# Kernel tuning notes

Hardware: AMD Instinct MI355X
Metric: run time of the kernel (lower is better)

The kernel has to match this reference:

```python
import jax, jax.numpy as jnp
import numpy as np

B, S, HID = 1, 2048, 2048
H, KVH, D = 16, 8, 128
QR, KR, VR = 6, 2, 2
SOFTCAP = 50.0
SCALING = D ** -0.5
NEG = -1e9


def _rope(Bfac, cos, sin):
    # Bfac: [b, s, r, d]; cos/sin: [s, d//2]; rotates adjacent pairs (complex view)
    x = Bfac.reshape(*Bfac.shape[:-1], D // 2, 2)
    xe, xo = x[..., 0], x[..., 1]
    c = cos[None, :, None, :]
    s = sin[None, :, None, :]
    oe = xe * c - xo * s
    oo = xe * s + xo * c
    return jnp.stack([oe, oo], axis=-1).reshape(Bfac.shape)


def setup_inputs() -> dict:
    key = jax.random.key(0)
    ks = jax.random.split(key, 12)
    hidden_states = jax.random.normal(ks[0], (B, S, HID), jnp.float32)
    # rotary tables (standard RoPE frequencies)
    inv_freq = 1.0 / (10000.0 ** (jnp.arange(0, D, 2, dtype=jnp.float32) / D))
    t = jnp.arange(S, dtype=jnp.float32)
    ang = t[:, None] * inv_freq[None, :]            # [S, D//2]
    cos, sin = jnp.cos(ang), jnp.sin(ang)
    # causal additive mask [1,1,S,S]
    causal = jnp.tril(jnp.ones((S, S), bool))
    mask = jnp.where(causal, 0.0, NEG).astype(jnp.float32)[None, None]
    kv_write_indices = jnp.arange(S, dtype=jnp.int32)
    sc = lambda k, shp: jax.random.normal(k, shp, jnp.float32) * (shp[0] ** -0.5)
    return {
        "hidden_states": hidden_states, "cos": cos, "sin": sin, "mask": mask,
        "kv_write_indices": kv_write_indices,
        "WAq": sc(ks[1], (HID, H * QR)), "WAk": sc(ks[2], (HID, KVH * KR)),
        "WAv": sc(ks[3], (HID, KVH * VR)), "WBq": sc(ks[4], (HID, QR * D)),
        "WBk": sc(ks[5], (HID, KR * D)), "WBv": sc(ks[6], (HID, VR * D)),
        "Wo": sc(ks[7], (H * D, HID)),
    }


def reference(hidden_states, cos, sin, mask, kv_write_indices,
              WAq, WAk, WAv, WBq, WBk, WBv, Wo):
    b, s, _ = hidden_states.shape
    # factor projections (never materialize full Q/K/V)
    A_q = (hidden_states @ WAq).reshape(b, s, H, QR)
    A_k = (hidden_states @ WAk).reshape(b, s, KVH, KR)
    A_v = (hidden_states @ WAv).reshape(b, s, KVH, VR)
    B_q = (hidden_states @ WBq).reshape(b, s, QR, D)
    B_k = (hidden_states @ WBk).reshape(b, s, KR, D)
    B_v = (hidden_states @ WBv).reshape(b, s, VR, D)
    # RoPE on B factors
    B_q = _rope(B_q, cos, sin)
    B_k = _rope(B_k, cos, sin)
    # prefill: kv_write_indices = arange(S) => cache slices equal current factors
    # GQA: broadcast KV heads up to H
    hpk = H // KVH
    A_k = jnp.repeat(A_k, hpk, axis=2)   # [b,k,H,KR]
    A_v = jnp.repeat(A_v, hpk, axis=2)   # [b,k,H,VR]
    # factor-expanded attention scores
    B_dots = jnp.einsum('bqrd,bksd->bqkrs', B_q, B_k) * SCALING
    attn = jnp.einsum('bqhr,bkhs,bqkrs->bhqk', A_q, A_k, B_dots)
    # logit softcapping
    attn = SOFTCAP * jnp.tanh(attn / SOFTCAP)
    attn = attn + mask
    probs = jax.nn.softmax(attn.astype(jnp.float32), axis=-1).astype(hidden_states.dtype)
    # factor-expanded output
    out = jnp.einsum('bhqk,bkhu,bkud->bhqd', probs, A_v, B_v)
    out = out.transpose(0, 2, 1, 3).reshape(b, s, H * D)
    return out @ Wo
```

## Files before the change

### kernel.cpp

```cpp
#include <hip/hip_runtime.h>


constexpr int SEQ   = 2048;
constexpr int HIDN  = 2048;
constexpr int NHEAD = 16;
constexpr int NKVH  = 8;
constexpr int DH    = 128;
constexpr int NCOLS = 1408;

typedef __bf16 bf16x8 __attribute__((ext_vector_type(8)));
typedef float  f32x4  __attribute__((ext_vector_type(4)));

#define MFMA(a, b, c) __builtin_amdgcn_mfma_f32_16x16x32_bf16((a), (b), (c), 0, 0, 0)

__device__ __forceinline__ void gload_lds16(const void* g, void* l) {
  __builtin_amdgcn_global_load_lds(
      (const __attribute__((address_space(1))) void*)g,
      (__attribute__((address_space(3))) void*)l, 16, 0, 0);
}


__global__ __launch_bounds__(256) void k_prep(
    const float* __restrict__ hidden,
    const float* __restrict__ WAq, const float* __restrict__ WAk,
    const float* __restrict__ WAv, const float* __restrict__ WBq,
    const float* __restrict__ WBk, const float* __restrict__ WBv,
    const float* __restrict__ Wo,
    __bf16* __restrict__ hid_bf, __bf16* __restrict__ WT,
    __bf16* __restrict__ WoT) {
  const int bid = blockIdx.x;
  if (bid < 2048) {
    const int i = (bid * 256 + threadIdx.x) * 8;
    f32x4 a = *(const f32x4*)(hidden + i);
    f32x4 b = *(const f32x4*)(hidden + i + 4);
    bf16x8 v;
#pragma unroll
    for (int j = 0; j < 4; j++) { v[j] = (__bf16)a[j]; v[4 + j] = (__bf16)b[j]; }
    *(bf16x8*)(hid_bf + i) = v;
  } else if (bid < 2048 + 44 * 64) {
    const int t = bid - 2048;
    const int bc = (t % 44) * 32, bk = (t / 44) * 32;
    __shared__ float tl[32][33];
    const int tx = threadIdx.x & 31, ty = threadIdx.x >> 5;
    const int c = bc + tx;
#pragma unroll
    for (int j = 0; j < 32; j += 8) {
      const int k = bk + ty + j;
      float v;
      if (c < 96)        v = WAq[k * 96 + c];
      else if (c < 112)  v = WAk[k * 16 + (c - 96)];
      else if (c < 128)  v = WAv[k * 16 + (c - 112)];
      else if (c < 896)  v = WBq[k * 768 + (c - 128)];
      else if (c < 1152) v = WBk[k * 256 + (c - 896)];
      else               v = WBv[k * 256 + (c - 1152)];
      tl[ty + j][tx] = v;
    }
    __syncthreads();
#pragma unroll
    for (int j = 0; j < 32; j += 8)
      WT[(size_t)(bc + ty + j) * HIDN + bk + tx] = (__bf16)tl[tx][ty + j];
  } else {
    const int t = bid - (2048 + 44 * 64);
    const int bn = (t % 64) * 32, bk = (t / 64) * 32;
    __shared__ float tl[32][33];
    const int tx = threadIdx.x & 31, ty = threadIdx.x >> 5;
#pragma unroll
    for (int j = 0; j < 32; j += 8)
      tl[ty + j][tx] = Wo[(size_t)(bk + ty + j) * HIDN + bn + tx];
    __syncthreads();
#pragma unroll
    for (int j = 0; j < 32; j += 8)
      WoT[(size_t)(bn + ty + j) * HIDN + bk + tx] = (__bf16)tl[tx][ty + j];
  }
}


__global__ __launch_bounds__(256) void k_gemm_bt(const __bf16* __restrict__ A,
                                                 const __bf16* __restrict__ BT,
                                                 float* __restrict__ C,
                                                 int M, int N, int K) {
  __shared__ __bf16 As[4][4096];
  __shared__ __bf16 Bs[4][2048];
  const int tid = threadIdx.x;
  const int w = tid >> 6, lane = tid & 63;
  const int lhi = lane >> 4, llo = lane & 15;
  const int wr = w >> 1, wc = w & 1;

  const int nx = gridDim.x, ny = gridDim.y;
  const int id = blockIdx.y * nx + blockIdx.x;
  int brow, bcol;
  if (((ny & 1) == 0) && ((nx & 3) == 0)) {
    const int g = id & 7, k = id >> 3;
    const int rows = ny >> 1, cols = nx >> 2;
    const int rg = g >> 2, cg = g & 3;
    const int r = k % rows, c = k / rows;
    brow = (rg * rows + r) * 128;
    bcol = (cg * cols + c) * 64;
  } else {
    const int cpx = (nx * ny) >> 3;
    const int sid = (id & 7) * cpx + (id >> 3);
    brow = (sid / nx) * 128;
    bcol = (sid % nx) * 64;
  }

  const int rA = lane >> 2, kA = (lane & 3) * 8;
  const int nt = K >> 5;

  f32x4 acc[4][2];
#pragma unroll
  for (int m = 0; m < 4; m++)
#pragma unroll
    for (int n = 0; n < 2; n++) acc[m][n] = (f32x4){0.f, 0.f, 0.f, 0.f};

  auto stage = [&](int t) {
    const int buf = t & 3;
    const int k0 = t * 32;
#pragma unroll
    for (int i = 0; i < 2; i++) {
      int seg = w * 2 + i;
      int row = seg * 16 + rA;
      gload_lds16(A + (size_t)(brow + row) * K + k0 + kA, &As[buf][seg * 512]);
    }
    gload_lds16(BT + (size_t)(bcol + w * 16 + rA) * K + k0 + kA, &Bs[buf][w * 512]);
  };

  stage(0); stage(1); stage(2);
  asm volatile("s_waitcnt vmcnt(6)" ::: "memory");
  __builtin_amdgcn_s_barrier();

  for (int t = 0; t < nt; t++) {
    if (t + 3 < nt) stage(t + 3);
    const int buf = t & 3;
    bf16x8 af[4], bfr[2];
#pragma unroll
    for (int m = 0; m < 4; m++)
      af[m] = *(const bf16x8*)&As[buf][(wr * 64 + m * 16 + llo) * 32 + lhi * 8];
#pragma unroll
    for (int n = 0; n < 2; n++)
      bfr[n] = *(const bf16x8*)&Bs[buf][(wc * 32 + n * 16 + llo) * 32 + lhi * 8];
#pragma unroll
    for (int m = 0; m < 4; m++)
#pragma unroll
      for (int n = 0; n < 2; n++) acc[m][n] = MFMA(af[m], bfr[n], acc[m][n]);
    const int rem = nt - 2 - t;
    if (rem >= 2)      asm volatile("s_waitcnt vmcnt(6)" ::: "memory");
    else if (rem == 1) asm volatile("s_waitcnt vmcnt(3)" ::: "memory");
    else               asm volatile("s_waitcnt vmcnt(0)" ::: "memory");
    __builtin_amdgcn_s_barrier();
  }

#pragma unroll
  for (int m = 0; m < 4; m++)
#pragma unroll
    for (int n = 0; n < 2; n++) {
      int r0 = brow + wr * 64 + m * 16 + lhi * 4;
      int c0 = bcol + wc * 32 + n * 16 + llo;
#pragma unroll
      for (int r = 0; r < 4; r++) C[(size_t)(r0 + r) * N + c0] = acc[m][n][r];
    }
}


__global__ __launch_bounds__(128) void k_build_qkv(const float* __restrict__ P,
                                                   const float* __restrict__ cosT,
                                                   const float* __restrict__ sinT,
                                                   __bf16* __restrict__ Qo,
                                                   __bf16* __restrict__ Ko,
                                                   __bf16* __restrict__ Vto) {
  const int q = blockIdx.x, d = threadIdx.x;
  __shared__ float Ash[128];
  const float* row = P + (size_t)q * NCOLS;
  Ash[d] = row[d];
  __syncthreads();
  const int m2 = (d >> 1) * 2;
  const bool odd = d & 1;
  const float c = cosT[q * 64 + (d >> 1)];
  const float s = sinT[q * 64 + (d >> 1)];

  float qacc[16];
#pragma unroll
  for (int h = 0; h < 16; h++) qacc[h] = 0.f;
#pragma unroll
  for (int r = 0; r < 6; r++) {
    float xe = row[128 + r * 128 + m2];
    float xo = row[128 + r * 128 + m2 + 1];
    float br = odd ? (xe * s + xo * c) : (xe * c - xo * s);
#pragma unroll
    for (int h = 0; h < 16; h++) qacc[h] += Ash[h * 6 + r] * br;
  }
#pragma unroll
  for (int h = 0; h < 16; h++)
    Qo[((size_t)h * SEQ + q) * DH + d] = (__bf16)(qacc[h] * 0.08838834764831845f);

  float kacc[8];
#pragma unroll
  for (int g = 0; g < 8; g++) kacc[g] = 0.f;
#pragma unroll
  for (int ss = 0; ss < 2; ss++) {
    float xe = row[896 + ss * 128 + m2];
    float xo = row[896 + ss * 128 + m2 + 1];
    float bs = odd ? (xe * s + xo * c) : (xe * c - xo * s);
#pragma unroll
    for (int g = 0; g < 8; g++) kacc[g] += Ash[96 + g * 2 + ss] * bs;
  }
#pragma unroll
  for (int g = 0; g < 8; g++)
    Ko[((size_t)g * SEQ + q) * DH + d] = (__bf16)kacc[g];

  float vacc[8];
#pragma unroll
  for (int g = 0; g < 8; g++) vacc[g] = 0.f;
#pragma unroll
  for (int u = 0; u < 2; u++) {
    float vu = row[1152 + u * 128 + d];
#pragma unroll
    for (int g = 0; g < 8; g++) vacc[g] += Ash[112 + g * 2 + u] * vu;
  }
#pragma unroll
  for (int g = 0; g < 8; g++)
    Vto[((size_t)g * DH + d) * SEQ + q] = (__bf16)vacc[g];
}


__global__ __launch_bounds__(256) void k_attn(const __bf16* __restrict__ Q,
                                              const __bf16* __restrict__ Kc,
                                              const __bf16* __restrict__ Vt,
                                              float* __restrict__ AOf0,
                                              float* __restrict__ AOf1,
                                              float* __restrict__ Ls) {
  const int raw = blockIdx.x;
  const int g = raw & 7;
  const int j = raw >> 3;
  const int bqi = 31 - (j >> 2);
  const int hh = (j >> 1) & 1;
  const int p = j & 1;
  const int h = g * 2 + hh;
  const int w = threadIdx.x >> 6, lane = threadIdx.x & 63;
  const int lhi = lane >> 4, llo = lane & 15;
  const int q0 = bqi * 64 + w * 16;
  const int t0 = p * (bqi + 1), t1 = t0 + bqi + 1;

  __shared__ __bf16 KVs[2][8192];
  __shared__ __bf16 Plds[4][512];

  const __bf16* Qh = Q  + (size_t)h * SEQ * DH;
  const __bf16* Kg = Kc + (size_t)g * SEQ * DH;
  const __bf16* Vg = Vt + (size_t)g * DH * SEQ;
  __bf16* Pl = Plds[w];
  float* AOc = p ? AOf1 : AOf0;

  bf16x8 aq[4];
#pragma unroll
  for (int c = 0; c < 4; c++)
    aq[c] = *(const bf16x8*)&Qh[(size_t)(q0 + llo) * DH + c * 32 + lhi * 8];

  f32x4 oacc[8];
  float lsum[4] = {0.f, 0.f, 0.f, 0.f};
#pragma unroll
  for (int n = 0; n < 8; n++) oacc[n] = (f32x4){0.f, 0.f, 0.f, 0.f};

  auto stage = [&](int kb, int buf) {
    __bf16* L = KVs[buf];
    if (w < 2) {
#pragma unroll
      for (int u = 0; u < 4; u++) {
        int c = w * 256 + u * 64 + lane;
        int row = c >> 4, jj = c & 15;
        gload_lds16(Kg + (size_t)(kb + row) * DH + ((jj ^ (row & 7)) * 8),
                    L + (w * 256 + u * 64) * 8);
      }
    } else {
#pragma unroll
      for (int u = 0; u < 4; u++) {
        int c = (w - 2) * 256 + u * 64 + lane;
        int d = c >> 2, jj = c & 3;
        gload_lds16(Vg + (size_t)d * SEQ + kb + ((jj ^ ((d >> 1) & 3)) * 8),
                    L + 4096 + ((w - 2) * 256 + u * 64) * 8);
      }
    }
  };

  stage(t0 * 32, t0 & 1);
  for (int t = t0; t < t1; t++) {
    const int kb = t * 32;
    const int buf = t & 1;
    if (t + 1 < t1) {
      stage(kb + 32, buf ^ 1);
      asm volatile("s_waitcnt vmcnt(4)" ::: "memory");
    } else {
      asm volatile("s_waitcnt vmcnt(0)" ::: "memory");
    }
    __builtin_amdgcn_s_barrier();
    if (kb <= q0 + 15) {
      const __bf16* Kl = KVs[buf];
      const __bf16* Vl = KVs[buf] + 4096;
      f32x4 s0 = {0.f, 0.f, 0.f, 0.f}, s1 = {0.f, 0.f, 0.f, 0.f};
#pragma unroll
      for (int c = 0; c < 4; c++) {
        const int row0 = llo, row1 = 16 + llo;
        bf16x8 k0 = *(const bf16x8*)((const char*)Kl + row0 * 256 +
                                     ((c * 64 + lhi * 16) ^ ((row0 & 7) << 4)));
        bf16x8 k1 = *(const bf16x8*)((const char*)Kl + row1 * 256 +
                                     ((c * 64 + lhi * 16) ^ ((row1 & 7) << 4)));
        s0 = MFMA(aq[c], k0, s0);
        s1 = MFMA(aq[c], k1, s1);
      }
#pragma unroll
      for (int r = 0; r < 4; r++) {
        const int qrow = q0 + lhi * 4 + r;
        const int rho = lhi * 4 + r;
        float t0e = exp2f(s0[r] * 0.057707802f);
        float t1e = exp2f(s1[r] * 0.057707802f);
        float p0 = exp2f(72.134752f - 144.269504f * __builtin_amdgcn_rcpf(t0e + 1.f));
        float p1 = exp2f(72.134752f - 144.269504f * __builtin_amdgcn_rcpf(t1e + 1.f));
        if (kb + llo > qrow) p0 = 0.f;
        if (kb + 16 + llo > qrow) p1 = 0.f;
        lsum[r] += p0 + p1;
        const int sw = ((rho >> 1) & 3) << 4;
        *(__bf16*)((char*)Pl + rho * 64 + ((llo * 2) ^ sw))      = (__bf16)p0;
        *(__bf16*)((char*)Pl + rho * 64 + ((llo * 2 + 32) ^ sw)) = (__bf16)p1;
      }
      bf16x8 pa = *(const bf16x8*)((const char*)Pl + llo * 64 +
                                   ((lhi * 16) ^ (((llo >> 1) & 3) << 4)));
#pragma unroll
      for (int n = 0; n < 8; n++) {
        const int d = n * 16 + llo;
        bf16x8 vf = *(const bf16x8*)((const char*)Vl + d * 64 +
                                     ((lhi * 16) ^ (((d >> 1) & 3) << 4)));
        oacc[n] = MFMA(pa, vf, oacc[n]);
      }
    }
    asm volatile("" ::: "memory");
    __builtin_amdgcn_s_barrier();
  }

#pragma unroll
  for (int r = 0; r < 4; r++) {
    float tsum = lsum[r];
    tsum += __shfl_xor(tsum, 1);
    tsum += __shfl_xor(tsum, 2);
    tsum += __shfl_xor(tsum, 4);
    tsum += __shfl_xor(tsum, 8);
    const int qrow = q0 + lhi * 4 + r;
    if (llo == 0) Ls[((size_t)p * NHEAD + h) * SEQ + qrow] = tsum;
#pragma unroll
    for (int n = 0; n < 8; n++)
      AOc[(size_t)qrow * HIDN + h * DH + n * 16 + llo] = oacc[n][r];
  }
}


__global__ __launch_bounds__(256) void k_norm(const float* __restrict__ A0,
                                              const float* __restrict__ A1,
                                              const float* __restrict__ Ls,
                                              __bf16* __restrict__ AO) {
  const int i = (blockIdx.x * 256 + threadIdx.x) * 4;
  const int q = i >> 11, h = (i & 2047) >> 7;
  const float inv = 1.f / (Ls[h * SEQ + q] + Ls[(NHEAD + h) * SEQ + q]);
  f32x4 a = *(const f32x4*)(A0 + i);
  f32x4 b = *(const f32x4*)(A1 + i);
#pragma unroll
  for (int j = 0; j < 4; j++) AO[i + j] = (__bf16)((a[j] + b[j]) * inv);
}


extern "C" void kernel_launch(void* const* d_in, const int* in_sizes, int n_in,
                              void* d_out, int out_size, void* d_ws, size_t ws_size,
                              hipStream_t stream) {
  const float* hidden = (const float*)d_in[0];
  const float* cosT   = (const float*)d_in[1];
  const float* sinT   = (const float*)d_in[2];
  const float* WAq = (const float*)d_in[5];
  const float* WAk = (const float*)d_in[6];
  const float* WAv = (const float*)d_in[7];
  const float* WBq = (const float*)d_in[8];
  const float* WBk = (const float*)d_in[9];
  const float* WBv = (const float*)d_in[10];
  const float* Wo  = (const float*)d_in[11];
  float* out = (float*)d_out;

  char* ws = (char*)d_ws;
  __bf16* hid_bf = (__bf16*)(ws);
  __bf16* WallT  = (__bf16*)(ws + 8388608);
  float*  Pproj  = (float*)(ws + 14155776);
  __bf16* WoT    = (__bf16*)(ws + 25690112);
  __bf16* Qb     = (__bf16*)(ws + 34078720);
  __bf16* Kb     = (__bf16*)(ws + 42467328);
  __bf16* Vt     = (__bf16*)(ws + 46661632);
  float*  AOf0   = (float*)(ws);
  float*  AOf1   = (float*)(ws + 50855936);
  float*  Ls     = (float*)(ws + 67633152);
  __bf16* AO     = (__bf16*)(ws + 34078720);

  k_prep<<<2048 + 44 * 64 + 64 * 64, 256, 0, stream>>>(
      hidden, WAq, WAk, WAv, WBq, WBk, WBv, Wo, hid_bf, WallT, WoT);
  k_gemm_bt<<<dim3(NCOLS / 64, SEQ / 128), 256, 0, stream>>>(hid_bf, WallT, Pproj,
                                                             SEQ, NCOLS, HIDN);
  k_build_qkv<<<SEQ, 128, 0, stream>>>(Pproj, cosT, sinT, Qb, Kb, Vt);
  k_attn<<<1024, 256, 0, stream>>>(Qb, Kb, Vt, AOf0, AOf1, Ls);
  k_norm<<<(SEQ * HIDN / 4) / 256, 256, 0, stream>>>(AOf0, AOf1, Ls, AO);
  k_gemm_bt<<<dim3(HIDN / 64, SEQ / 128), 256, 0, stream>>>(AO, WoT, out,
                                                            SEQ, HIDN, HIDN);
}
```

Before: 160.8 us.

## Compute transposed scores to feed P into PV MFMA from registers

Swaps the MFMA operands in the QK^T step so each lane holds scores for one query row across key positions. The softmax probabilities can then be packed directly into the A-operand register layout for the PV MFMA, which removes the per-wave LDS round trip for P. The V fragment loads are rearranged into two 8-byte reads per lane to match the permuted key order. The causal mask is applied only on diagonal tiles, and the row-sum reduction needs fewer shuffles. This relies on the key permutation being consistent between the P and V fragments.

```diff
diff --git a/kernel.cpp b/kernel.cpp
--- a/kernel.cpp
+++ b/kernel.cpp
@@ -241,12 +241,10 @@
   const int t0 = p * (bqi + 1), t1 = t0 + bqi + 1;
 
   __shared__ __bf16 KVs[2][8192];
-  __shared__ __bf16 Plds[4][512];
 
   const __bf16* Qh = Q  + (size_t)h * SEQ * DH;
   const __bf16* Kg = Kc + (size_t)g * SEQ * DH;
   const __bf16* Vg = Vt + (size_t)g * DH * SEQ;
-  __bf16* Pl = Plds[w];
   float* AOc = p ? AOf1 : AOf0;
 
   bf16x8 aq[4];
@@ -255,9 +253,13 @@
     aq[c] = *(const bf16x8*)&Qh[(size_t)(q0 + llo) * DH + c * 32 + lhi * 8];
 
   f32x4 oacc[8];
-  float lsum[4] = {0.f, 0.f, 0.f, 0.f};
+  float lsum = 0.f;
 #pragma unroll
   for (int n = 0; n < 8; n++) oacc[n] = (f32x4){0.f, 0.f, 0.f, 0.f};
+
+  const int swv = (llo >> 1) & 3;
+  const int vb0 = ((((lhi >> 1) ^ swv) << 4) | ((lhi & 1) << 3)) + llo * 64;
+  const int vb1 = (((((lhi >> 1) + 2) ^ swv) << 4) | ((lhi & 1) << 3)) + llo * 64;
 
   auto stage = [&](int kb, int buf) {
     __bf16* L = KVs[buf];
@@ -292,57 +294,61 @@
     }
     __builtin_amdgcn_s_barrier();
     if (kb <= q0 + 15) {
-      const __bf16* Kl = KVs[buf];
-      const __bf16* Vl = KVs[buf] + 4096;
+      const char* Kl = (const char*)KVs[buf];
+      const char* Vl = (const char*)(KVs[buf] + 4096);
       f32x4 s0 = {0.f, 0.f, 0.f, 0.f}, s1 = {0.f, 0.f, 0.f, 0.f};
 #pragma unroll
       for (int c = 0; c < 4; c++) {
         const int row0 = llo, row1 = 16 + llo;
-        bf16x8 k0 = *(const bf16x8*)((const char*)Kl + row0 * 256 +
+        bf16x8 k0 = *(const bf16x8*)(Kl + row0 * 256 +
                                      ((c * 64 + lhi * 16) ^ ((row0 & 7) << 4)));
-        bf16x8 k1 = *(const bf16x8*)((const char*)Kl + row1 * 256 +
+        bf16x8 k1 = *(const bf16x8*)(Kl + row1 * 256 +
                                      ((c * 64 + lhi * 16) ^ ((row1 & 7) << 4)));
-        s0 = MFMA(aq[c], k0, s0);
-        s1 = MFMA(aq[c], k1, s1);
-      }
+        s0 = MFMA(k0, aq[c], s0);
+        s1 = MFMA(k1, aq[c], s1);
+      }
+      float e[8];
 #pragma unroll
       for (int r = 0; r < 4; r++) {
-        const int qrow = q0 + lhi * 4 + r;
-        const int rho = lhi * 4 + r;
-        float t0e = exp2f(s0[r] * 0.057707802f);
-        float t1e = exp2f(s1[r] * 0.057707802f);
-        float p0 = exp2f(72.134752f - 144.269504f * __builtin_amdgcn_rcpf(t0e + 1.f));
-        float p1 = exp2f(72.134752f - 144.269504f * __builtin_amdgcn_rcpf(t1e + 1.f));
-        if (kb + llo > qrow) p0 = 0.f;
-        if (kb + 16 + llo > qrow) p1 = 0.f;
-        lsum[r] += p0 + p1;
-        const int sw = ((rho >> 1) & 3) << 4;
-        *(__bf16*)((char*)Pl + rho * 64 + ((llo * 2) ^ sw))      = (__bf16)p0;
-        *(__bf16*)((char*)Pl + rho * 64 + ((llo * 2 + 32) ^ sw)) = (__bf16)p1;
-      }
-      bf16x8 pa = *(const bf16x8*)((const char*)Pl + llo * 64 +
-                                   ((lhi * 16) ^ (((llo >> 1) & 3) << 4)));
+        float a0 = exp2f(s0[r] * 0.057707802f);
+        float a1 = exp2f(s1[r] * 0.057707802f);
+        e[r]     = exp2f(72.134752f - 144.269504f * __builtin_amdgcn_rcpf(a0 + 1.f));
+        e[4 + r] = exp2f(72.134752f - 144.269504f * __builtin_amdgcn_rcpf(a1 + 1.f));
+      }
+      if (kb + 31 > q0) {
+        const int qrow = q0 + llo;
+#pragma unroll
+        for (int r = 0; r < 4; r++) {
+          if (kb + lhi * 4 + r > qrow)      e[r] = 0.f;
+          if (kb + 16 + lhi * 4 + r > qrow) e[4 + r] = 0.f;
+        }
+      }
+#pragma unroll
+      for (int r = 0; r < 4; r++) lsum += e[r] + e[4 + r];
+      union { bf16x8 v8; unsigned u[4]; } pu;
+      asm("v_cvt_pk_bf16_f32 %0, %1, %2" : "=v"(pu.u[0]) : "v"(e[0]), "v"(e[1]));
+      asm("v_cvt_pk_bf16_f32 %0, %1, %2" : "=v"(pu.u[1]) : "v"(e[2]), "v"(e[3]));
+      asm("v_cvt_pk_bf16_f32 %0, %1, %2" : "=v"(pu.u[2]) : "v"(e[4]), "v"(e[5]));
+      asm("v_cvt_pk_bf16_f32 %0, %1, %2" : "=v"(pu.u[3]) : "v"(e[6]), "v"(e[7]));
 #pragma unroll
       for (int n = 0; n < 8; n++) {
-        const int d = n * 16 + llo;
-        bf16x8 vf = *(const bf16x8*)((const char*)Vl + d * 64 +
-                                     ((lhi * 16) ^ (((d >> 1) & 3) << 4)));
-        oacc[n] = MFMA(pa, vf, oacc[n]);
+        union { bf16x8 v8; struct { uint2 lo, hi; } d; } vu;
+        vu.d.lo = *(const uint2*)(Vl + vb0 + n * 1024);
+        vu.d.hi = *(const uint2*)(Vl + vb1 + n * 1024);
+        oacc[n] = MFMA(pu.v8, vu.v8, oacc[n]);
       }
     }
     asm volatile("" ::: "memory");
     __builtin_amdgcn_s_barrier();
   }
 
+  float tsum = lsum;
+  tsum += __shfl_xor(tsum, 16);
+  tsum += __shfl_xor(tsum, 32);
+  if (lhi == 0) Ls[((size_t)p * NHEAD + h) * SEQ + q0 + llo] = tsum;
 #pragma unroll
   for (int r = 0; r < 4; r++) {
-    float tsum = lsum[r];
-    tsum += __shfl_xor(tsum, 1);
-    tsum += __shfl_xor(tsum, 2);
-    tsum += __shfl_xor(tsum, 4);
-    tsum += __shfl_xor(tsum, 8);
     const int qrow = q0 + lhi * 4 + r;
-    if (llo == 0) Ls[((size_t)p * NHEAD + h) * SEQ + qrow] = tsum;
 #pragma unroll
     for (int n = 0; n < 8; n++)
       AOc[(size_t)qrow * HIDN + h * DH + n * 16 + llo] = oacc[n][r];
```

Result: no change. 161.6 us (+0.5%).
